# Kernel optimization log

Hardware: AMD Instinct MI355X
Metric: run time of the kernel (lower is better)

Reference implementation:

```python
import jax, jax.numpy as jnp
import numpy as np

DIM = 1024
NUM_HEADS = 16
HEAD_DIM = DIM // NUM_HEADS  # 64
H = 32
W = 32
NREG = 8
B = 8
N = H * W + NREG  # 1032


def setup_inputs() -> dict:
    key = jax.random.key(0)
    ks = jax.random.split(key, 6)
    def rn(k, shape, std):
        return jax.random.normal(k, shape, dtype=jnp.float32) * std
    return {
        "x": rn(ks[0], (B, N, DIM), 1.0),
        "qkv_w": rn(ks[1], (3 * DIM, DIM), 0.02),
        "qkv_b": jnp.zeros((3 * DIM,), jnp.float32),
        "proj_w": rn(ks[2], (DIM, DIM), 0.02),
        "proj_b": jnp.zeros((DIM,), jnp.float32),
        "rel_pos_h": rn(ks[3], (2 * H - 1, HEAD_DIM), 0.02),
        "rel_pos_w": rn(ks[4], (2 * W - 1, HEAD_DIM), 0.02),
        "nreg": NREG,
        "cait": 0,
    }


def _rel_pos_table(rel_pos, size):
    # q_size == k_size == size -> relative index = i - j + (size - 1)
    coords = jnp.arange(size)[:, None] - jnp.arange(size)[None, :] + (size - 1)
    return rel_pos[coords]  # (size, size, head_dim)


def reference(x, qkv_w, qkv_b, proj_w, proj_b, rel_pos_h, rel_pos_w, nreg, cait):
    Bx, Nx, C = x.shape
    hd = C // NUM_HEADS
    scale = hd ** (-0.5)
    # qkv: (B, N, 3, nH, hd) -> (3, nH, B, N, hd) -> (3, nH*B, N, hd)
    qkv = (x @ qkv_w.T + qkv_b).reshape(Bx, Nx, 3, NUM_HEADS, hd)
    qkv = jnp.transpose(qkv, (2, 3, 0, 1, 4)).reshape(3, NUM_HEADS * Bx, Nx, hd)
    q, k, v = qkv[0], qkv[1], qkv[2]
    if cait:
        q = q[:, -nreg:]
    attn = jnp.einsum('bqd,bkd->bqk', q * scale, k)  # (nH*B, Nq, N)
    if not cait:
        hw = H * W
        Rh = _rel_pos_table(rel_pos_h, H)  # (H, H, hd)
        Rw = _rel_pos_table(rel_pos_w, W)  # (W, W, hd)
        r_q = q[:, :hw].reshape(-1, H, W, hd)  # unscaled q, grid tokens only
        rel_h = jnp.einsum('bhwc,hkc->bhwk', r_q, Rh)
        rel_w = jnp.einsum('bhwc,wkc->bhwk', r_q, Rw)
        grid = (attn[:, :hw, :hw].reshape(-1, H, W, H, W)
                + rel_h[:, :, :, :, None] + rel_w[:, :, :, None, :])
        attn = attn.at[:, :hw, :hw].set(grid.reshape(-1, hw, hw))
    attn = jax.nn.softmax(attn, axis=-1)
    out = jnp.einsum('bqk,bkd->bqd', attn, v)  # (nH*B, Nq, hd)
    out = out.reshape(NUM_HEADS, Bx, -1, hd)
    out = jnp.transpose(out, (1, 2, 0, 3)).reshape(Bx, -1, C)
    return out @ proj_w.T + proj_b
```

## Files before the change

### kernel.cpp

```cpp
#include <hip/hip_runtime.h>

#define BATCH 8
#define NTOK 1032
#define NPAD 1152
#define MTOT (BATCH*NTOK)
#define MPAD 8320

#define SCALE_Q 0.18033688011112042f
#define C2      5.770780163555854f

typedef __bf16 bf16x8 __attribute__((ext_vector_type(8)));
typedef float f32x4 __attribute__((ext_vector_type(4)));
typedef unsigned short us8 __attribute__((ext_vector_type(8)));
typedef unsigned short us4 __attribute__((ext_vector_type(4)));
typedef short s4 __attribute__((ext_vector_type(4)));

__device__ __forceinline__ unsigned short f2bf(float f){
  unsigned int u = __builtin_bit_cast(unsigned int, f);
  u += 0x7fffu + ((u >> 16) & 1u);
  return (unsigned short)(u >> 16);
}
__device__ __forceinline__ float bf2f(unsigned short u){
  return __builtin_bit_cast(float, (unsigned int)u << 16);
}

#define MFMA16(a,b,c) __builtin_amdgcn_mfma_f32_16x16x32_bf16( \
    __builtin_bit_cast(bf16x8,(a)), __builtin_bit_cast(bf16x8,(b)), (c), 0, 0, 0)
#define MFMAH(a,b,c) __builtin_amdgcn_mfma_f32_16x16x16bf16_1k( \
    __builtin_bit_cast(s4,(a)), __builtin_bit_cast(s4,(b)), (c), 0, 0, 0)

__device__ __forceinline__ void gl_lds16(const unsigned short* g, unsigned short* l){
  __builtin_amdgcn_global_load_lds(
      (const __attribute__((address_space(1))) unsigned int*)g,
      (__attribute__((address_space(3))) unsigned int*)l, 16, 0, 0);
}

__global__ __launch_bounds__(256) void cvt_f32_bf16(const float* __restrict__ in,
                                                    unsigned short* __restrict__ out, int n4){
  int i = blockIdx.x * 256 + threadIdx.x;
  if (i < n4){
    float4 v = reinterpret_cast<const float4*>(in)[i];
    us4 o; o.x = f2bf(v.x); o.y = f2bf(v.y); o.z = f2bf(v.z); o.w = f2bf(v.w);
    reinterpret_cast<us4*>(out)[i] = o;
  }
}

__global__ __launch_bounds__(256) void pad_zero(unsigned short* __restrict__ qb,
                                                unsigned short* __restrict__ kb,
                                                unsigned short* __restrict__ xb,
                                                unsigned short* __restrict__ ao){
  int i = blockIdx.x * 256 + threadIdx.x;
  const int t1 = 128 * (NPAD - NTOK) * 64;
  const int t2 = t1 + (MPAD - MTOT) * 1024;
  const int t3 = t2 + (MPAD - MTOT) * 1024;
  if (i < t1){
    int bh = i / ((NPAD - NTOK) * 64);
    int r  = (i / 64) % (NPAD - NTOK);
    int d  = i % 64;
    int idx = (bh * NPAD + NTOK + r) * 64 + d;
    qb[idx] = 0;
    kb[idx] = 0;
  } else if (i < t2){
    xb[(size_t)MTOT * 1024 + (i - t1)] = 0;
  } else if (i < t3){
    ao[(size_t)MTOT * 1024 + (i - t2)] = 0;
  }
}

__global__ __launch_bounds__(256,3) void qkv_gemm(
    const unsigned short* __restrict__ A,
    const unsigned short* __restrict__ Bw,
    const float* __restrict__ bias,
    unsigned short* __restrict__ qb,
    unsigned short* __restrict__ kb,
    unsigned short* __restrict__ vb)
{
  const int K = 1024;
  __shared__ __align__(16) unsigned short As[3][128*32];
  __shared__ __align__(16) unsigned short Bs[3][128*32];
  int tid = threadIdx.x;
  int id = blockIdx.x;
  int work = (id & 7) * 195 + (id >> 3);
  int m0 = (work / 24) * 128, n0 = (work % 24) * 128;
  int w = tid >> 6, lane = tid & 63, lr = lane & 15, lg = lane >> 4;
  int wr = w >> 1, wc = w & 1;
  int srow = lane >> 2;
  int scol = ((lane & 3) ^ ((lane >> 3) & 3)) * 8;
  int sa = (lg ^ ((lr >> 1) & 3)) * 8;
  f32x4 acc[4][4] = {};

  auto stage = [&](int buf, int k0){
    #pragma unroll
    for (int i = 0; i < 2; i++){
      int q = w * 2 + i;
      gl_lds16(&A [(size_t)(m0 + q*16 + srow) * K + k0 + scol], &As[buf][q*512]);
      gl_lds16(&Bw[(size_t)(n0 + q*16 + srow) * K + k0 + scol], &Bs[buf][q*512]);
    }
  };

  stage(0, 0);
  stage(1, 32);

  for (int kt = 0; kt < 32; kt++){
    int cur = kt % 3;
    if (kt < 30){
      stage((kt + 2) % 3, (kt + 2) * 32);
      asm volatile("s_waitcnt vmcnt(8)" ::: "memory");
    } else if (kt == 30){
      asm volatile("s_waitcnt vmcnt(4)" ::: "memory");
    } else {
      asm volatile("s_waitcnt vmcnt(0)" ::: "memory");
    }
    __builtin_amdgcn_sched_barrier(0);
    __builtin_amdgcn_s_barrier();

    us8 a[4], b[4];
    #pragma unroll
    for (int mi = 0; mi < 4; mi++) a[mi] = *reinterpret_cast<const us8*>(&As[cur][(wr*64 + mi*16 + lr)*32 + sa]);
    #pragma unroll
    for (int ni = 0; ni < 4; ni++) b[ni] = *reinterpret_cast<const us8*>(&Bs[cur][(wc*64 + ni*16 + lr)*32 + sa]);
    __builtin_amdgcn_s_setprio(1);
    #pragma unroll
    for (int mi = 0; mi < 4; mi++)
      #pragma unroll
      for (int ni = 0; ni < 4; ni++)
        acc[mi][ni] = MFMA16(a[mi], b[ni], acc[mi][ni]);
    __builtin_amdgcn_s_setprio(0);
    __builtin_amdgcn_s_barrier();
  }

  #pragma unroll
  for (int mi = 0; mi < 4; mi++){
    #pragma unroll
    for (int ni = 0; ni < 4; ni++){
      #pragma unroll
      for (int reg = 0; reg < 4; reg++){
        int m = m0 + wr*64 + mi*16 + lg*4 + reg;
        if (m >= MTOT) continue;
        int n = n0 + wc*64 + ni*16 + lr;
        float val = acc[mi][ni][reg] + bias[n];
        int b_ = m / NTOK, nidx = m % NTOK;
        int t = n >> 10, h = (n >> 6) & 15, d = n & 63;
        int bh = h * BATCH + b_;
        if (t == 0){
          qb[(size_t)(bh * NPAD + nidx) * 64 + d] = f2bf(val * SCALE_Q);
        } else if (t == 1){
          kb[(size_t)(bh * NPAD + nidx) * 64 + d] = f2bf(val);
        } else {
          vb[(size_t)(bh * NTOK + nidx) * 64 + d] = f2bf(val);
        }
      }
    }
  }
}

__global__ __launch_bounds__(256) void transpose_v(const unsigned short* __restrict__ vb,
                                                   unsigned short* __restrict__ vt){
  __shared__ unsigned short Ls[64][72];
  int blk = blockIdx.x;
  int bh = blk / 17, tl = blk % 17;
  int n0 = tl * 64;
  int t = threadIdx.x;

  #pragma unroll
  for (int p = 0; p < 2; p++){
    int idx = p * 256 + t;
    int r = idx >> 3, c = idx & 7;
    us8 v = {};
    if (n0 + r < NTOK)
      v = *reinterpret_cast<const us8*>(&vb[((size_t)bh * NTOK + n0 + r) * 64 + c * 8]);
    *reinterpret_cast<us8*>(&Ls[r][c * 8]) = v;
  }
  __syncthreads();

  int d = t & 63, ng = t >> 6;
  us8 o[2];
  #pragma unroll
  for (int hf = 0; hf < 2; hf++){
    #pragma unroll
    for (int j = 0; j < 8; j++) o[hf][j] = Ls[ng*16 + hf*8 + j][d];
    *reinterpret_cast<us8*>(&vt[((size_t)bh * 64 + d) * NPAD + n0 + ng*16 + hf*8]) = o[hf];
  }
}

__global__ __launch_bounds__(256,3) void attn_kernel(
    const unsigned short* __restrict__ qb,
    const unsigned short* __restrict__ kb,
    const unsigned short* __restrict__ vt,
    const float* __restrict__ rph,
    const float* __restrict__ rpw,
    unsigned short* __restrict__ ao)
{
  __shared__ __align__(16) unsigned short Ks[2][64*64];
  __shared__ __align__(16) unsigned short Vs[2][64*64];
  __shared__ unsigned short RHt[32*128];
  __shared__ unsigned short RWc[32*128];

  int id = blockIdx.x;
  int work = (id & 7) * 144 + (id >> 3);
  int bh = work / 9;
  int qt = work % 9;
  int tid = threadIdx.x, w = tid >> 6, lane = tid & 63, lr = lane & 15, lg = lane >> 4;
  int h = bh >> 3, b_ = bh & 7;

  const unsigned short* qbase = qb + (size_t)bh * NPAD * 64;
  const unsigned short* kbase = kb + (size_t)bh * NPAD * 64;
  const unsigned short* vbase = vt + (size_t)bh * 64 * NPAD;

  #pragma unroll
  for (int t = 0; t < 2; t++){
    int i = t*256 + tid;
    int row = i >> 3, cs = (i & 7) ^ (row & 7);
    gl_lds16(&kbase[(size_t)row*64 + cs*8],   &Ks[0][(t*256 + w*64)*8]);
    gl_lds16(&vbase[(size_t)row*NPAD + cs*8], &Vs[0][(t*256 + w*64)*8]);
  }

  us8 aq[2][2];
  #pragma unroll
  for (int qf = 0; qf < 2; qf++){
    int qrow = qt*128 + w*32 + qf*16 + lr;
    aq[qf][0] = *reinterpret_cast<const us8*>(&qbase[(size_t)qrow*64 + lg*8]);
    aq[qf][1] = *reinterpret_cast<const us8*>(&qbase[(size_t)qrow*64 + 32 + lg*8]);
  }

  float rwreg[2][2][4] = {};

  if (qt < 8){
    int qh = qt*4 + w;
    f32x4 accH[2][2] = {};
    #pragma unroll
    for (int ks = 0; ks < 2; ks++){
      #pragma unroll
      for (int nf2 = 0; nf2 < 2; nf2++){
        int t = nf2*16 + lr;
        const float* src = rph + (size_t)(qh - t + 31)*64 + ks*32 + lg*8;
        us8 ar;
        #pragma unroll
        for (int j = 0; j < 8; j++) ar[j] = f2bf(src[j]);
        #pragma unroll
        for (int qf = 0; qf < 2; qf++) accH[qf][nf2] = MFMA16(ar, aq[qf][ks], accH[qf][nf2]);
      }
    }
    #pragma unroll
    for (int qf = 0; qf < 2; qf++)
      #pragma unroll
      for (int nf2 = 0; nf2 < 2; nf2++)
        #pragma unroll
        for (int reg = 0; reg < 4; reg++){
          int t_out = nf2*16 + lg*4 + reg;
          RHt[t_out*128 + w*32 + qf*16 + lr] = f2bf(accH[qf][nf2][reg] * 8.0f);
        }
    f32x4 accW[2][4] = {};
    #pragma unroll
    for (int ks = 0; ks < 2; ks++){
      #pragma unroll
      for (int nf = 0; nf < 4; nf++){
        int t = nf*16 + lr;
        us8 aw_ = {};
        if (t < 63){
          const float* src = rpw + (size_t)t*64 + ks*32 + lg*8;
          #pragma unroll
          for (int j = 0; j < 8; j++) aw_[j] = f2bf(src[j]);
        }
        #pragma unroll
        for (int qf = 0; qf < 2; qf++) accW[qf][nf] = MFMA16(aw_, aq[qf][ks], accW[qf][nf]);
      }
    }
    #pragma unroll
    for (int qf = 0; qf < 2; qf++)
      #pragma unroll
      for (int nf = 0; nf < 4; nf++)
        #pragma unroll
        for (int reg = 0; reg < 4; reg++){
          int t_out = nf*16 + lg*4 + reg;
          int qw = qf*16 + lr;
          int kw = qw - t_out + 31;
          if (kw >= 0 && kw < 32)
            RWc[kw*128 + w*32 + qf*16 + lr] = f2bf(accW[qf][nf][reg] * 8.0f);
        }
    #pragma unroll
    for (int qf = 0; qf < 2; qf++)
      #pragma unroll
      for (int hf = 0; hf < 2; hf++)
        #pragma unroll
        for (int reg = 0; reg < 4; reg++)
          rwreg[qf][hf][reg] = bf2f(RWc[(hf*16 + lg*4 + reg)*128 + w*32 + qf*16 + lr]);
  }
  __syncthreads();

  f32x4 O[2][4] = {};
  f32x4 lac[2] = {};
  s4 ones4;
  ones4.x = (short)0x3F80; ones4.y = (short)0x3F80; ones4.z = (short)0x3F80; ones4.w = (short)0x3F80;

  for (int kt = 0; kt < 17; kt++){
    int cur = kt & 1;
    if (kt < 16){
      #pragma unroll
      for (int t = 0; t < 2; t++){
        int i = t*256 + tid;
        int row = i >> 3, cs = (i & 7) ^ (row & 7);
        gl_lds16(&kbase[(size_t)((kt+1)*64 + row)*64 + cs*8], &Ks[cur^1][(t*256 + w*64)*8]);
        gl_lds16(&vbase[(size_t)row*NPAD + (kt+1)*64 + cs*8], &Vs[cur^1][(t*256 + w*64)*8]);
      }
      asm volatile("s_waitcnt vmcnt(4)" ::: "memory");
    } else {
      asm volatile("s_waitcnt vmcnt(0)" ::: "memory");
    }
    __builtin_amdgcn_sched_barrier(0);
    __builtin_amdgcn_s_barrier();

    f32x4 S[2][4] = {};
    __builtin_amdgcn_s_setprio(1);
    #pragma unroll
    for (int ks = 0; ks < 2; ks++)
      #pragma unroll
      for (int nf = 0; nf < 4; nf++){
        us8 bk = *reinterpret_cast<const us8*>(
            &Ks[cur][(nf*16 + lr)*64 + (((ks*4 + lg) ^ (lr & 7)) * 8)]);
        S[0][nf] = MFMA16(bk, aq[0][ks], S[0][nf]);
        S[1][nf] = MFMA16(bk, aq[1][ks], S[1][nf]);
      }
    __builtin_amdgcn_s_setprio(0);

    bool gk = (qt < 8) && (kt < 16);
    float rh2[2][2];
    #pragma unroll
    for (int qf = 0; qf < 2; qf++)
      #pragma unroll
      for (int hf = 0; hf < 2; hf++)
        rh2[qf][hf] = gk ? (bf2f(RHt[(kt*2 + hf)*128 + w*32 + qf*16 + lr]) - C2) : -C2;

    s4 pa[2][4];
    #pragma unroll
    for (int qf = 0; qf < 2; qf++){
      #pragma unroll
      for (int nf = 0; nf < 4; nf++){
        float pv[4];
        #pragma unroll
        for (int reg = 0; reg < 4; reg++){
          float logit = S[qf][nf][reg] + rh2[qf][nf>>1] + (gk ? rwreg[qf][nf&1][reg] : 0.f);
          float p = __builtin_amdgcn_exp2f(logit);
          int key = kt*64 + nf*16 + lg*4 + reg;
          pv[reg] = (key < NTOK) ? p : 0.f;
        }
        unsigned int u0 = __builtin_amdgcn_perm(
            __builtin_bit_cast(unsigned int, pv[1]), __builtin_bit_cast(unsigned int, pv[0]), 0x07060302u);
        unsigned int u1 = __builtin_amdgcn_perm(
            __builtin_bit_cast(unsigned int, pv[3]), __builtin_bit_cast(unsigned int, pv[2]), 0x07060302u);
        uint2 uu; uu.x = u0; uu.y = u1;
        pa[qf][nf] = __builtin_bit_cast(s4, uu);
      }
    }

    __builtin_amdgcn_s_setprio(1);
    #pragma unroll
    for (int qf = 0; qf < 2; qf++)
      #pragma unroll
      for (int nf = 0; nf < 4; nf++)
        lac[qf] = MFMAH(pa[qf][nf], ones4, lac[qf]);
    #pragma unroll
    for (int nf = 0; nf < 4; nf++){
      #pragma unroll
      for (int nfd = 0; nfd < 4; nfd++){
        us4 bv = *reinterpret_cast<const us4*>(
            &Vs[cur][(nfd*16 + lr)*64 + (((nf*2 + (lg>>1)) ^ (lr & 7))*8) + (lg&1)*4]);
        O[0][nfd] = MFMAH(pa[0][nf], bv, O[0][nfd]);
        O[1][nfd] = MFMAH(pa[1][nf], bv, O[1][nfd]);
      }
    }
    __builtin_amdgcn_s_setprio(0);
    __builtin_amdgcn_s_barrier();
  }

  #pragma unroll
  for (int qf = 0; qf < 2; qf++)
    #pragma unroll
    for (int reg = 0; reg < 4; reg++){
      int qg = qt*128 + w*32 + qf*16 + lg*4 + reg;
      if (qg < NTOK){
        float inv = 1.0f / lac[qf][reg];
        #pragma unroll
        for (int nfd = 0; nfd < 4; nfd++)
          ao[(size_t)(b_ * NTOK + qg) * 1024 + h*64 + nfd*16 + lr] = f2bf(O[qf][nfd][reg] * inv);
      }
    }
}

__global__ __launch_bounds__(256,3) void proj_gemm(
    const unsigned short* __restrict__ A,
    const unsigned short* __restrict__ Bw,
    const float* __restrict__ bias,
    float* __restrict__ out)
{
  const int K = 1024;
  __shared__ __align__(16) unsigned short As[3][128*32];
  __shared__ __align__(16) unsigned short Bs[3][128*32];
  int tid = threadIdx.x;
  int id = blockIdx.x;
  int work = (id & 7) * 65 + (id >> 3);
  int m0 = (work / 8) * 128, n0 = (work % 8) * 128;
  int w = tid >> 6, lane = tid & 63, lr = lane & 15, lg = lane >> 4;
  int wr = w >> 1, wc = w & 1;
  int srow = lane >> 2;
  int scol = ((lane & 3) ^ ((lane >> 3) & 3)) * 8;
  int sa = (lg ^ ((lr >> 1) & 3)) * 8;
  f32x4 acc[4][4] = {};

  auto stage = [&](int buf, int k0){
    #pragma unroll
    for (int i = 0; i < 2; i++){
      int q = w * 2 + i;
      gl_lds16(&A [(size_t)(m0 + q*16 + srow) * K + k0 + scol], &As[buf][q*512]);
      gl_lds16(&Bw[(size_t)(n0 + q*16 + srow) * K + k0 + scol], &Bs[buf][q*512]);
    }
  };

  stage(0, 0);
  stage(1, 32);

  for (int kt = 0; kt < 32; kt++){
    int cur = kt % 3;
    if (kt < 30){
      stage((kt + 2) % 3, (kt + 2) * 32);
      asm volatile("s_waitcnt vmcnt(8)" ::: "memory");
    } else if (kt == 30){
      asm volatile("s_waitcnt vmcnt(4)" ::: "memory");
    } else {
      asm volatile("s_waitcnt vmcnt(0)" ::: "memory");
    }
    __builtin_amdgcn_sched_barrier(0);
    __builtin_amdgcn_s_barrier();

    us8 a[4], b[4];
    #pragma unroll
    for (int mi = 0; mi < 4; mi++) a[mi] = *reinterpret_cast<const us8*>(&As[cur][(wr*64 + mi*16 + lr)*32 + sa]);
    #pragma unroll
    for (int ni = 0; ni < 4; ni++) b[ni] = *reinterpret_cast<const us8*>(&Bs[cur][(wc*64 + ni*16 + lr)*32 + sa]);
    __builtin_amdgcn_s_setprio(1);
    #pragma unroll
    for (int mi = 0; mi < 4; mi++)
      #pragma unroll
      for (int ni = 0; ni < 4; ni++)
        acc[mi][ni] = MFMA16(a[mi], b[ni], acc[mi][ni]);
    __builtin_amdgcn_s_setprio(0);
    __builtin_amdgcn_s_barrier();
  }

  #pragma unroll
  for (int mi = 0; mi < 4; mi++){
    #pragma unroll
    for (int ni = 0; ni < 4; ni++){
      #pragma unroll
      for (int reg = 0; reg < 4; reg++){
        int m = m0 + wr*64 + mi*16 + lg*4 + reg;
        if (m >= MTOT) continue;
        int n = n0 + wc*64 + ni*16 + lr;
        out[(size_t)m * 1024 + n] = acc[mi][ni][reg] + bias[n];
      }
    }
  }
}

extern "C" void kernel_launch(void* const* d_in, const int* in_sizes, int n_in,
                              void* d_out, int out_size, void* d_ws, size_t ws_size,
                              hipStream_t stream)
{
  const float* x      = (const float*)d_in[0];
  const float* qkv_w  = (const float*)d_in[1];
  const float* qkv_b  = (const float*)d_in[2];
  const float* proj_w = (const float*)d_in[3];
  const float* proj_b = (const float*)d_in[4];
  const float* rph    = (const float*)d_in[5];
  const float* rpw    = (const float*)d_in[6];
  float* out = (float*)d_out;

  char* ws = (char*)d_ws;
  size_t off = 0;
  auto alloc = [&](size_t bytes){ char* p = ws + off; off += (bytes + 255) & ~(size_t)255; return p; };
  unsigned short* x_bf  = (unsigned short*)alloc((size_t)MPAD * 1024 * 2);
  unsigned short* qw_bf = (unsigned short*)alloc((size_t)3072 * 1024 * 2);
  unsigned short* pw_bf = (unsigned short*)alloc((size_t)1024 * 1024 * 2);
  unsigned short* qbuf  = (unsigned short*)alloc((size_t)128 * NPAD * 64 * 2);
  unsigned short* kbuf  = (unsigned short*)alloc((size_t)128 * NPAD * 64 * 2);
  unsigned short* vtbuf = (unsigned short*)alloc((size_t)128 * 64 * NPAD * 2);
  unsigned short* aout  = (unsigned short*)alloc((size_t)MPAD * 1024 * 2);
  if (off > ws_size) return;

  unsigned short* vbuf = aout;

  int n4x = MTOT * 1024 / 4;
  cvt_f32_bf16<<<dim3((n4x + 255) / 256), 256, 0, stream>>>(x, x_bf, n4x);
  int n4q = 3072 * 1024 / 4;
  cvt_f32_bf16<<<dim3((n4q + 255) / 256), 256, 0, stream>>>(qkv_w, qw_bf, n4q);
  int n4p = 1024 * 1024 / 4;
  cvt_f32_bf16<<<dim3((n4p + 255) / 256), 256, 0, stream>>>(proj_w, pw_bf, n4p);

  int npad = 128 * (NPAD - NTOK) * 64 + 2 * (MPAD - MTOT) * 1024;
  pad_zero<<<dim3((npad + 255) / 256), 256, 0, stream>>>(qbuf, kbuf, x_bf, aout);

  qkv_gemm<<<dim3(1560), 256, 0, stream>>>(x_bf, qw_bf, qkv_b, qbuf, kbuf, vbuf);
  transpose_v<<<dim3(128 * 17), 256, 0, stream>>>(vbuf, vtbuf);
  attn_kernel<<<dim3(1152), 256, 0, stream>>>(qbuf, kbuf, vtbuf, rph, rpw, aout);
  proj_gemm<<<dim3(520), 256, 0, stream>>>(aout, pw_bf, proj_b, out);
}
```

Baseline: 254.0 us.

## Fuse prep kernels and retile GEMMs to 256x128 with 512-thread double buffering

Merges the three fp32-to-bf16 conversion launches and the padding-zero launch into one prep kernel to cut launch count. Both the QKV and projection GEMMs move from 128x128 tiles with 256 threads and triple buffering to 256x128 tiles with 512 threads (8 waves) and double buffering. MPAD grows to a multiple of 256 so the larger M tiles stay in bounds. This should raise operand reuse per tile and lower LDS use per block, but the shallower pipeline may expose more load latency and fewer blocks cover the grid.

```diff
diff --git a/kernel.cpp b/kernel.cpp
--- a/kernel.cpp
+++ b/kernel.cpp
@@ -4,7 +4,7 @@
 #define NTOK 1032
 #define NPAD 1152
 #define MTOT (BATCH*NTOK)
-#define MPAD 8320
+#define MPAD 8448
 
 #define SCALE_Q 0.18033688011112042f
 #define C2      5.770780163555854f
@@ -35,39 +35,46 @@
       (__attribute__((address_space(3))) unsigned int*)l, 16, 0, 0);
 }
 
-__global__ __launch_bounds__(256) void cvt_f32_bf16(const float* __restrict__ in,
-                                                    unsigned short* __restrict__ out, int n4){
+__global__ __launch_bounds__(256) void prep(
+    const float* __restrict__ x, const float* __restrict__ qw, const float* __restrict__ pw,
+    unsigned short* __restrict__ x_bf, unsigned short* __restrict__ qw_bf,
+    unsigned short* __restrict__ pw_bf,
+    unsigned short* __restrict__ qb, unsigned short* __restrict__ kb,
+    unsigned short* __restrict__ ao)
+{
   int i = blockIdx.x * 256 + threadIdx.x;
-  if (i < n4){
-    float4 v = reinterpret_cast<const float4*>(in)[i];
-    us4 o; o.x = f2bf(v.x); o.y = f2bf(v.y); o.z = f2bf(v.z); o.w = f2bf(v.w);
-    reinterpret_cast<us4*>(out)[i] = o;
-  }
-}
-
-__global__ __launch_bounds__(256) void pad_zero(unsigned short* __restrict__ qb,
-                                                unsigned short* __restrict__ kb,
-                                                unsigned short* __restrict__ xb,
-                                                unsigned short* __restrict__ ao){
-  int i = blockIdx.x * 256 + threadIdx.x;
-  const int t1 = 128 * (NPAD - NTOK) * 64;
+  const int n4x = MTOT * 1024 / 4;
+  const int n4q = 3072 * 1024 / 4;
+  const int n4p = 1024 * 1024 / 4;
+  const int c1 = n4x, c2 = c1 + n4q, c3 = c2 + n4p;
+  const int t1 = c3 + 128 * (NPAD - NTOK) * 64;
   const int t2 = t1 + (MPAD - MTOT) * 1024;
   const int t3 = t2 + (MPAD - MTOT) * 1024;
-  if (i < t1){
-    int bh = i / ((NPAD - NTOK) * 64);
-    int r  = (i / 64) % (NPAD - NTOK);
-    int d  = i % 64;
+
+  if (i < c3){
+    const float* src; unsigned short* dst; int j;
+    if (i < c1){ src = x;  dst = x_bf;  j = i; }
+    else if (i < c2){ src = qw; dst = qw_bf; j = i - c1; }
+    else { src = pw; dst = pw_bf; j = i - c2; }
+    float4 v = reinterpret_cast<const float4*>(src)[j];
+    us4 o; o.x = f2bf(v.x); o.y = f2bf(v.y); o.z = f2bf(v.z); o.w = f2bf(v.w);
+    reinterpret_cast<us4*>(dst)[j] = o;
+  } else if (i < t1){
+    int j = i - c3;
+    int bh = j / ((NPAD - NTOK) * 64);
+    int r  = (j / 64) % (NPAD - NTOK);
+    int d  = j % 64;
     int idx = (bh * NPAD + NTOK + r) * 64 + d;
     qb[idx] = 0;
     kb[idx] = 0;
   } else if (i < t2){
-    xb[(size_t)MTOT * 1024 + (i - t1)] = 0;
+    x_bf[(size_t)MTOT * 1024 + (i - t1)] = 0;
   } else if (i < t3){
     ao[(size_t)MTOT * 1024 + (i - t2)] = 0;
   }
 }
 
-__global__ __launch_bounds__(256,3) void qkv_gemm(
+__global__ __launch_bounds__(512,4) void qkv_gemm(
     const unsigned short* __restrict__ A,
     const unsigned short* __restrict__ Bw,
     const float* __restrict__ bias,
@@ -76,12 +83,12 @@
     unsigned short* __restrict__ vb)
 {
   const int K = 1024;
-  __shared__ __align__(16) unsigned short As[3][128*32];
-  __shared__ __align__(16) unsigned short Bs[3][128*32];
+  __shared__ __align__(16) unsigned short As[2][256*32];
+  __shared__ __align__(16) unsigned short Bs[2][128*32];
   int tid = threadIdx.x;
   int id = blockIdx.x;
-  int work = (id & 7) * 195 + (id >> 3);
-  int m0 = (work / 24) * 128, n0 = (work % 24) * 128;
+  int work = (id & 7) * 99 + (id >> 3);
+  int m0 = (work / 24) * 256, n0 = (work % 24) * 128;
   int w = tid >> 6, lane = tid & 63, lr = lane & 15, lg = lane >> 4;
   int wr = w >> 1, wc = w & 1;
   int srow = lane >> 2;
@@ -90,24 +97,18 @@
   f32x4 acc[4][4] = {};
 
   auto stage = [&](int buf, int k0){
-    #pragma unroll
-    for (int i = 0; i < 2; i++){
-      int q = w * 2 + i;
-      gl_lds16(&A [(size_t)(m0 + q*16 + srow) * K + k0 + scol], &As[buf][q*512]);
-      gl_lds16(&Bw[(size_t)(n0 + q*16 + srow) * K + k0 + scol], &Bs[buf][q*512]);
-    }
+    gl_lds16(&A [(size_t)(m0 + w*32      + srow) * K + k0 + scol], &As[buf][(w*2  )*512]);
+    gl_lds16(&A [(size_t)(m0 + w*32 + 16 + srow) * K + k0 + scol], &As[buf][(w*2+1)*512]);
+    gl_lds16(&Bw[(size_t)(n0 + w*16      + srow) * K + k0 + scol], &Bs[buf][ w      *512]);
   };
 
   stage(0, 0);
-  stage(1, 32);
 
   for (int kt = 0; kt < 32; kt++){
-    int cur = kt % 3;
-    if (kt < 30){
-      stage((kt + 2) % 3, (kt + 2) * 32);
-      asm volatile("s_waitcnt vmcnt(8)" ::: "memory");
-    } else if (kt == 30){
-      asm volatile("s_waitcnt vmcnt(4)" ::: "memory");
+    int cur = kt & 1;
+    if (kt < 31){
+      stage(cur ^ 1, (kt + 1) * 32);
+      asm volatile("s_waitcnt vmcnt(3)" ::: "memory");
     } else {
       asm volatile("s_waitcnt vmcnt(0)" ::: "memory");
     }
@@ -387,19 +388,19 @@
     }
 }
 
-__global__ __launch_bounds__(256,3) void proj_gemm(
+__global__ __launch_bounds__(512,4) void proj_gemm(
     const unsigned short* __restrict__ A,
     const unsigned short* __restrict__ Bw,
     const float* __restrict__ bias,
     float* __restrict__ out)
 {
   const int K = 1024;
-  __shared__ __align__(16) unsigned short As[3][128*32];
-  __shared__ __align__(16) unsigned short Bs[3][128*32];
+  __shared__ __align__(16) unsigned short As[2][256*32];
+  __shared__ __align__(16) unsigned short Bs[2][128*32];
   int tid = threadIdx.x;
   int id = blockIdx.x;
-  int work = (id & 7) * 65 + (id >> 3);
-  int m0 = (work / 8) * 128, n0 = (work % 8) * 128;
+  int work = (id & 7) * 33 + (id >> 3);
+  int m0 = (work / 8) * 256, n0 = (work % 8) * 128;
   int w = tid >> 6, lane = tid & 63, lr = lane & 15, lg = lane >> 4;
   int wr = w >> 1, wc = w & 1;
   int srow = lane >> 2;
@@ -408,24 +409,18 @@
   f32x4 acc[4][4] = {};
 
   auto stage = [&](int buf, int k0){
-    #pragma unroll
-    for (int i = 0; i < 2; i++){
-      int q = w * 2 + i;
-      gl_lds16(&A [(size_t)(m0 + q*16 + srow) * K + k0 + scol], &As[buf][q*512]);
-      gl_lds16(&Bw[(size_t)(n0 + q*16 + srow) * K + k0 + scol], &Bs[buf][q*512]);
-    }
+    gl_lds16(&A [(size_t)(m0 + w*32      + srow) * K + k0 + scol], &As[buf][(w*2  )*512]);
+    gl_lds16(&A [(size_t)(m0 + w*32 + 16 + srow) * K + k0 + scol], &As[buf][(w*2+1)*512]);
+    gl_lds16(&Bw[(size_t)(n0 + w*16      + srow) * K + k0 + scol], &Bs[buf][ w      *512]);
   };
 
   stage(0, 0);
-  stage(1, 32);
 
   for (int kt = 0; kt < 32; kt++){
-    int cur = kt % 3;
-    if (kt < 30){
-      stage((kt + 2) % 3, (kt + 2) * 32);
-      asm volatile("s_waitcnt vmcnt(8)" ::: "memory");
-    } else if (kt == 30){
-      asm volatile("s_waitcnt vmcnt(4)" ::: "memory");
+    int cur = kt & 1;
+    if (kt < 31){
+      stage(cur ^ 1, (kt + 1) * 32);
+      asm volatile("s_waitcnt vmcnt(3)" ::: "memory");
     } else {
       asm volatile("s_waitcnt vmcnt(0)" ::: "memory");
     }
@@ -489,18 +484,14 @@
 
   unsigned short* vbuf = aout;
 
-  int n4x = MTOT * 1024 / 4;
-  cvt_f32_bf16<<<dim3((n4x + 255) / 256), 256, 0, stream>>>(x, x_bf, n4x);
-  int n4q = 3072 * 1024 / 4;
-  cvt_f32_bf16<<<dim3((n4q + 255) / 256), 256, 0, stream>>>(qkv_w, qw_bf, n4q);
-  int n4p = 1024 * 1024 / 4;
-  cvt_f32_bf16<<<dim3((n4p + 255) / 256), 256, 0, stream>>>(proj_w, pw_bf, n4p);
-
-  int npad = 128 * (NPAD - NTOK) * 64 + 2 * (MPAD - MTOT) * 1024;
-  pad_zero<<<dim3((npad + 255) / 256), 256, 0, stream>>>(qbuf, kbuf, x_bf, aout);
-
-  qkv_gemm<<<dim3(1560), 256, 0, stream>>>(x_bf, qw_bf, qkv_b, qbuf, kbuf, vbuf);
+  const int n4x = MTOT * 1024 / 4, n4q = 3072 * 1024 / 4, n4p = 1024 * 1024 / 4;
+  int ntot = n4x + n4q + n4p + 128 * (NPAD - NTOK) * 64 + 2 * (MPAD - MTOT) * 1024;
+  prep<<<dim3((ntot + 255) / 256), 256, 0, stream>>>(x, qkv_w, proj_w,
+                                                     x_bf, qw_bf, pw_bf,
+                                                     qbuf, kbuf, aout);
+
+  qkv_gemm<<<dim3(792), 512, 0, stream>>>(x_bf, qw_bf, qkv_b, qbuf, kbuf, vbuf);
   transpose_v<<<dim3(128 * 17), 256, 0, stream>>>(vbuf, vtbuf);
   attn_kernel<<<dim3(1152), 256, 0, stream>>>(qbuf, kbuf, vtbuf, rph, rpw, aout);
-  proj_gemm<<<dim3(520), 256, 0, stream>>>(aout, pw_bf, proj_b, out);
-}
+  proj_gemm<<<dim3(264), 512, 0, stream>>>(aout, pw_bf, proj_b, out);
+}
```

Result: faster. 226.9 us (-10.7%).
